# Kernel optimization log

Measured on AMD Instinct MI355X. Metric: run time of the kernel, lower is better.

The kernel has to match this reference:

```python
import jax, jax.numpy as jnp
import numpy as np

D = 1024
H = 16
HS = D // H
DFF = 4 * D
EPS = 1e-5


def setup_inputs() -> dict:
    key = jax.random.key(0)
    ks = jax.random.split(key, 16)
    s_attn = 1.0 / np.sqrt(D)
    x = jax.random.normal(ks[0], (4, 2048, D), dtype=jnp.float32)
    wq = jax.random.normal(ks[1], (H, D, HS), dtype=jnp.float32) * s_attn
    wk = jax.random.normal(ks[2], (H, D, HS), dtype=jnp.float32) * s_attn
    wv = jax.random.normal(ks[3], (H, D, HS), dtype=jnp.float32) * s_attn
    wo = jax.random.normal(ks[4], (D, D), dtype=jnp.float32) * s_attn
    bo = jnp.zeros((D,), dtype=jnp.float32)
    w1 = jax.random.normal(ks[5], (D, DFF), dtype=jnp.float32) * s_attn
    b1 = jnp.zeros((DFF,), dtype=jnp.float32)
    w2 = jax.random.normal(ks[6], (DFF, D), dtype=jnp.float32) * (1.0 / np.sqrt(DFF))
    b2 = jnp.zeros((D,), dtype=jnp.float32)
    g1 = jnp.ones((D,), dtype=jnp.float32)
    be1 = jnp.zeros((D,), dtype=jnp.float32)
    g2 = jnp.ones((D,), dtype=jnp.float32)
    be2 = jnp.zeros((D,), dtype=jnp.float32)
    return {"x": x, "wq": wq, "wk": wk, "wv": wv, "wo": wo, "bo": bo,
            "w1": w1, "b1": b1, "w2": w2, "b2": b2,
            "g1": g1, "be1": be1, "g2": g2, "be2": be2}


def _layernorm(x, g, b):
    mu = jnp.mean(x, axis=-1, keepdims=True)
    var = jnp.mean(jnp.square(x - mu), axis=-1, keepdims=True)
    return (x - mu) * jax.lax.rsqrt(var + EPS) * g + b


def _block(x, wq, wk, wv, wo, bo, w1, b1, w2, b2, g1, be1, g2, be2):
    B, T, C = x.shape
    h = _layernorm(x, g1, be1)
    q = jnp.einsum('btd,hdk->bhtk', h, wq)
    k = jnp.einsum('btd,hdk->bhtk', h, wk)
    v = jnp.einsum('btd,hdk->bhtk', h, wv)
    wei = jnp.einsum('bhtk,bhsk->bhts', q, k) * (HS ** -0.5)
    causal = jnp.tril(jnp.ones((T, T), dtype=bool))
    wei = jnp.where(causal, wei, -jnp.inf)
    wei = jax.nn.softmax(wei, axis=-1)
    attn = jnp.einsum('bhts,bhsk->bhtk', wei, v)  # (B,H,T,HS)
    attn = attn.transpose(0, 2, 1, 3).reshape(B, T, C)  # concat heads
    x = x + attn @ wo + bo
    h2 = _layernorm(x, g2, be2)
    ff = jax.nn.relu(h2 @ w1 + b1) @ w2 + b2
    return x + ff


def reference(x, wq, wk, wv, wo, bo, w1, b1, w2, b2, g1, be1, g2, be2):
    return _block(x, wq, wk, wv, wo, bo, w1, b1, w2, b2, g1, be1, g2, be2)
```

## Files before the change

kernel.cpp:

```cpp
#include <hip/hip_runtime.h>
#include <hip/hip_bf16.h>

#define D_ 1024
#define T_ 2048
#define B_ 4
#define H_ 16
#define HS_ 64
#define DFF_ 4096
#define M_TOT 8192

typedef short s8v __attribute__((ext_vector_type(8)));
typedef float f4v __attribute__((ext_vector_type(4)));

__device__ __forceinline__ void gll16(const void* g, void* l) {
  __builtin_amdgcn_global_load_lds(
      (__attribute__((address_space(1))) void*)(g),
      (__attribute__((address_space(3))) void*)(l), 16, 0, 0);
}

__device__ __forceinline__ short f2b(float f) {
  __hip_bfloat16 h = __float2bfloat16(f);
  short s; __builtin_memcpy(&s, &h, 2); return s;
}

#define VMCNT(N) asm volatile("s_waitcnt vmcnt(" #N ")" ::: "memory")
#define SBAR()  do { __builtin_amdgcn_s_barrier(); __builtin_amdgcn_sched_barrier(0); } while (0)

__global__ __launch_bounds__(256) void transpose_all_kernel(
    const float* __restrict__ wq, const float* __restrict__ wk,
    const float* __restrict__ wv, const float* __restrict__ wo,
    const float* __restrict__ w1, const float* __restrict__ w2,
    __hip_bfloat16* __restrict__ qkvT, __hip_bfloat16* __restrict__ woT,
    __hip_bfloat16* __restrict__ w1T, __hip_bfloat16* __restrict__ w2T) {
  const int bid = blockIdx.x;
  const float* src; __hip_bfloat16* dst;
  int R, C, rb, bx, by;
  if (bid < 3072) {
    int j = bid >> 10, w = bid & 1023;
    src = (j == 0) ? wq : (j == 1) ? wk : wv;
    dst = qkvT; R = 1024; C = 64;
    int z = w >> 6, xy = w & 63;
    bx = xy & 1; by = xy >> 1;
    src += (size_t)z * R * C;
    rb = j * 1024 + z * C;
  } else if (bid < 4096) {
    int w = bid - 3072;
    src = wo; dst = woT; R = 1024; C = 1024; rb = 0;
    bx = w & 31; by = w >> 5;
  } else if (bid < 8192) {
    int w = bid - 4096;
    src = w1; dst = w1T; R = 1024; C = 4096; rb = 0;
    bx = w & 127; by = w >> 7;
  } else {
    int w = bid - 8192;
    src = w2; dst = w2T; R = 4096; C = 1024; rb = 0;
    bx = w & 31; by = w >> 5;
  }
  __shared__ float tile[32][33];
  int c0 = bx * 32, r0 = by * 32;
  int tx = threadIdx.x, ty = threadIdx.y;
#pragma unroll
  for (int i = 0; i < 4; ++i)
    tile[ty + i * 8][tx] = src[(size_t)(r0 + ty + i * 8) * C + c0 + tx];
  __syncthreads();
#pragma unroll
  for (int i = 0; i < 4; ++i)
    dst[(size_t)(rb + c0 + ty + i * 8) * R + r0 + tx] =
        __float2bfloat16(tile[tx][ty + i * 8]);
}

__global__ __launch_bounds__(256) void transpose_v_kernel(
    const __hip_bfloat16* __restrict__ Vb, __hip_bfloat16* __restrict__ Vt) {
  const int bh = blockIdx.y;
  const int t0 = blockIdx.x * 64;
  __shared__ short tile[64][72];
  const int tid = threadIdx.x;
  const int r = tid >> 2, cg = tid & 3;
  const __hip_bfloat16* src = Vb + ((size_t)bh * T_ + t0 + r) * HS_ + cg * 16;
  s8v v0 = *(const s8v*)(src);
  s8v v1 = *(const s8v*)(src + 8);
  *(s8v*)&tile[r][cg * 16] = v0;
  *(s8v*)&tile[r][cg * 16 + 8] = v1;
  __syncthreads();
  const int hs = r;
  short o0[8], o1[8];
#pragma unroll
  for (int k2 = 0; k2 < 8; ++k2) o0[k2] = tile[cg * 16 + k2][hs];
#pragma unroll
  for (int k2 = 0; k2 < 8; ++k2) o1[k2] = tile[cg * 16 + 8 + k2][hs];
  __hip_bfloat16* dst = Vt + ((size_t)bh * HS_ + hs) * T_ + t0 + cg * 16;
  *(s8v*)dst = *(s8v*)o0;
  *(s8v*)(dst + 8) = *(s8v*)o1;
}

__global__ __launch_bounds__(256) void ln_kernel(
    const float* __restrict__ x, const float* __restrict__ g,
    const float* __restrict__ be, __hip_bfloat16* __restrict__ out) {
  int row = blockIdx.x;
  int t = threadIdx.x;
  float4 v = ((const float4*)(x + (size_t)row * D_))[t];
  float s = v.x + v.y + v.z + v.w;
  float ss = v.x * v.x + v.y * v.y + v.z * v.z + v.w * v.w;
#pragma unroll
  for (int o = 1; o < 64; o <<= 1) { s += __shfl_xor(s, o); ss += __shfl_xor(ss, o); }
  __shared__ float rs[4], rss[4];
  int w = t >> 6, l = t & 63;
  if (l == 0) { rs[w] = s; rss[w] = ss; }
  __syncthreads();
  s = rs[0] + rs[1] + rs[2] + rs[3];
  ss = rss[0] + rss[1] + rss[2] + rss[3];
  float mu = s * (1.f / D_);
  float var = ss * (1.f / D_) - mu * mu;
  float r = rsqrtf(var + 1e-5f);
  float4 gv = ((const float4*)g)[t];
  float4 bv = ((const float4*)be)[t];
  union { ushort4 u; __hip_bfloat16 h[4]; } pk;
  pk.h[0] = __float2bfloat16((v.x - mu) * r * gv.x + bv.x);
  pk.h[1] = __float2bfloat16((v.y - mu) * r * gv.y + bv.y);
  pk.h[2] = __float2bfloat16((v.z - mu) * r * gv.z + bv.z);
  pk.h[3] = __float2bfloat16((v.w - mu) * r * gv.w + bv.w);
  ((ushort4*)(out + (size_t)row * D_))[t] = pk.u;
}

__global__ __launch_bounds__(256) void gemm_bt_kernel(
    const __hip_bfloat16* __restrict__ A, const __hip_bfloat16* __restrict__ Bt,
    int M, int N, int K,
    float* __restrict__ p0, const float* __restrict__ bias,
    const float* __restrict__ res) {
  __shared__ short sA[2][128 * 32], sB[2][128 * 32];
  const int gdx = gridDim.x;
  const int nwg = gdx * gridDim.y;
  const int orig = blockIdx.y * gdx + blockIdx.x;
  const int xcd = orig & 7;
  const int c = orig >> 3;
  const int rows = (nwg >> 3) / gdx;
  const int i2 = c & 1;
  const int nn = (c >> 1) % gdx;
  const int gg = (c >> 1) / gdx;
  const int m0 = (xcd * rows + gg * 2 + i2) * 128, n0 = nn * 128;
  const int t = threadIdx.x, l = t & 63, w = t >> 6;
  const int wr = w >> 1, wc = w & 1, lg = l >> 4, lo = l & 15;
  f4v acc[4][4];
#pragma unroll
  for (int m = 0; m < 4; ++m)
#pragma unroll
    for (int n = 0; n < 4; ++n) acc[m][n] = (f4v){0.f, 0.f, 0.f, 0.f};
  const int NT = K >> 5;
  auto stage = [&](int kt, int bi) {
#pragma unroll
    for (int j = 0; j < 2; ++j) {
      int i = j * 256 + t;
      int row = i >> 2, sl = i & 3;
      int ss = sl ^ ((row >> 1) & 3);
      gll16(A + (size_t)(m0 + row) * K + kt * 32 + ss * 8, (char*)sA[bi] + i * 16);
      gll16(Bt + (size_t)(n0 + row) * K + kt * 32 + ss * 8, (char*)sB[bi] + i * 16);
    }
  };
  stage(0, 0);
  stage(1, 1);
  VMCNT(4);
  SBAR();
  for (int kt = 0; kt < NT; ++kt) {
    const int bi = kt & 1;
    s8v af[4], bf[4];
#pragma unroll
    for (int m = 0; m < 4; ++m) {
      int row = wr * 64 + m * 16 + lo;
      int ss = lg ^ ((row >> 1) & 3);
      af[m] = *(const s8v*)((const char*)sA[bi] + row * 64 + ss * 16);
    }
#pragma unroll
    for (int n = 0; n < 4; ++n) {
      int row = wc * 64 + n * 16 + lo;
      int ss = lg ^ ((row >> 1) & 3);
      bf[n] = *(const s8v*)((const char*)sB[bi] + row * 64 + ss * 16);
    }
    __builtin_amdgcn_s_setprio(1);
#pragma unroll
    for (int m = 0; m < 4; ++m)
#pragma unroll
      for (int n = 0; n < 4; ++n)
        acc[m][n] = __builtin_amdgcn_mfma_f32_16x16x32_bf16(af[m], bf[n], acc[m][n], 0, 0, 0);
    __builtin_amdgcn_s_setprio(0);
    if (kt == NT - 1) break;
    SBAR();
    if (kt + 2 < NT) { stage(kt + 2, bi); VMCNT(4); }
    else             { VMCNT(0); }
    SBAR();
  }
#pragma unroll
  for (int mi = 0; mi < 4; ++mi)
#pragma unroll
    for (int j = 0; j < 4; ++j) {
      int mg = m0 + wr * 64 + mi * 16 + lg * 4 + j;
#pragma unroll
      for (int ni = 0; ni < 4; ++ni) {
        int ng = n0 + wc * 64 + ni * 16 + lo;
        p0[(size_t)mg * N + ng] = res[(size_t)mg * N + ng] + acc[mi][ni][j] + bias[ng];
      }
    }
}

template <int EPI>
__global__ __launch_bounds__(512, 2) void gemm_bt_256(
    const __hip_bfloat16* __restrict__ A, const __hip_bfloat16* __restrict__ Bt,
    int M, int N, int K,
    void* __restrict__ p0, void* __restrict__ p1, void* __restrict__ p2,
    const float* __restrict__ bias) {
  __shared__ short sA[2][256 * 32], sB[2][256 * 32];
  const int gdx = gridDim.x;
  const int gdy = gridDim.y;
  const int orig = blockIdx.y * gdx + blockIdx.x;
  const int xcd = orig & 7;
  const int c = orig >> 3;
  const int rowsPerXcd = gdy >> 3;
  const int g = c / (2 * gdx);
  const int r = c % (2 * gdx);
  const int i2 = r & 1, nn = r >> 1;
  const int m0 = (xcd * rowsPerXcd + g * 2 + i2) * 256;
  const int n0 = nn * 256;
  const int t = threadIdx.x, l = t & 63, wid = t >> 6;
  const int wm = wid >> 2, wn = wid & 3, lg = l >> 4, lo = l & 15;
  f4v acc[8][4];
#pragma unroll
  for (int m = 0; m < 8; ++m)
#pragma unroll
    for (int n = 0; n < 4; ++n) acc[m][n] = (f4v){0.f, 0.f, 0.f, 0.f};
  const int NT = K >> 5;
  auto stage = [&](int kt, int bi) {
#pragma unroll
    for (int j = 0; j < 2; ++j) {
      int i = j * 512 + t;
      int row = i >> 2, sl = i & 3;
      int ss = sl ^ ((row >> 1) & 3);
      gll16(A + (size_t)(m0 + row) * K + kt * 32 + ss * 8, (char*)sA[bi] + i * 16);
      gll16(Bt + (size_t)(n0 + row) * K + kt * 32 + ss * 8, (char*)sB[bi] + i * 16);
    }
  };
  stage(0, 0);
  stage(1, 1);
  VMCNT(4);
  SBAR();
  for (int kt = 0; kt < NT; ++kt) {
    const int bi = kt & 1;
    const char* cA = (const char*)sA[bi];
    const char* cB = (const char*)sB[bi];
    s8v bf[4];
#pragma unroll
    for (int nr = 0; nr < 4; ++nr) {
      int row = wn * 64 + nr * 16 + lo;
      int ss = lg ^ ((row >> 1) & 3);
      bf[nr] = *(const s8v*)(cB + row * 64 + ss * 16);
    }
    {
      s8v af[4];
#pragma unroll
      for (int mr = 0; mr < 4; ++mr) {
        int row = wm * 128 + mr * 16 + lo;
        int ss = lg ^ ((row >> 1) & 3);
        af[mr] = *(const s8v*)(cA + row * 64 + ss * 16);
      }
      __builtin_amdgcn_s_setprio(1);
#pragma unroll
      for (int mr = 0; mr < 4; ++mr)
#pragma unroll
        for (int nr = 0; nr < 4; ++nr)
          acc[mr][nr] = __builtin_amdgcn_mfma_f32_16x16x32_bf16(af[mr], bf[nr], acc[mr][nr], 0, 0, 0);
      __builtin_amdgcn_s_setprio(0);
    }
    {
      s8v af[4];
#pragma unroll
      for (int mr = 0; mr < 4; ++mr) {
        int row = wm * 128 + (mr + 4) * 16 + lo;
        int ss = lg ^ ((row >> 1) & 3);
        af[mr] = *(const s8v*)(cA + row * 64 + ss * 16);
      }
      __builtin_amdgcn_s_setprio(1);
#pragma unroll
      for (int mr = 0; mr < 4; ++mr)
#pragma unroll
        for (int nr = 0; nr < 4; ++nr)
          acc[mr + 4][nr] = __builtin_amdgcn_mfma_f32_16x16x32_bf16(af[mr], bf[nr], acc[mr + 4][nr], 0, 0, 0);
      __builtin_amdgcn_s_setprio(0);
    }
    if (kt == NT - 1) break;
    SBAR();
    if (kt + 2 < NT) { stage(kt + 2, bi); VMCNT(4); }
    else             { VMCNT(0); }
    SBAR();
  }
#pragma unroll
  for (int mi = 0; mi < 8; ++mi)
#pragma unroll
    for (int j = 0; j < 4; ++j) {
      int mg = m0 + wm * 128 + mi * 16 + lg * 4 + j;
#pragma unroll
      for (int ni = 0; ni < 4; ++ni) {
        int ng = n0 + wn * 64 + ni * 16 + lo;
        float v = acc[mi][ni][j];
        if constexpr (EPI == 0) {
          int wi = ng >> 10, within = ng & 1023, hh = within >> 6, hs = within & 63;
          __hip_bfloat16* dst = (wi == 0) ? (__hip_bfloat16*)p0
                               : (wi == 1) ? (__hip_bfloat16*)p1
                                           : (__hip_bfloat16*)p2;
          int b = mg >> 11, tt = mg & 2047;
          dst[(((size_t)(b * H_ + hh)) * T_ + tt) * HS_ + hs] = __float2bfloat16(v);
        } else {
          float y = v + bias[ng];
          y = y > 0.f ? y : 0.f;
          ((__hip_bfloat16*)p0)[(size_t)mg * N + ng] = __float2bfloat16(y);
        }
      }
    }
}

template <bool MASK>
__device__ __forceinline__ void attn_step(
    int s0, int qrow, int lg, int lo,
    const short* __restrict__ sKb, const short* __restrict__ sVb,
    short* __restrict__ sPw,
    const s8v (&qf)[2][2], f4v (&acc)[2][4], float (&rsum)[2][4]) {
  s8v kf[4][2];
#pragma unroll
  for (int si = 0; si < 4; ++si) {
    int row = si * 16 + lo;
#pragma unroll
    for (int kc = 0; kc < 2; ++kc) {
      int slot = (kc * 4 + lg) ^ (row & 7);
      kf[si][kc] = *(const s8v*)((const char*)sKb + row * 128 + slot * 16);
    }
  }
  f4v sfr[2][4];
#pragma unroll
  for (int mi = 0; mi < 2; ++mi)
#pragma unroll
    for (int si = 0; si < 4; ++si) {
      sfr[mi][si] = (f4v){0.f, 0.f, 0.f, 0.f};
#pragma unroll
      for (int kc = 0; kc < 2; ++kc)
        sfr[mi][si] = __builtin_amdgcn_mfma_f32_16x16x32_bf16(
            qf[mi][kc], kf[si][kc], sfr[mi][si], 0, 0, 0);
    }
  const float c = 0.18033688f;
  float p[2][4][4];
#pragma unroll
  for (int mi = 0; mi < 2; ++mi)
#pragma unroll
    for (int si = 0; si < 4; ++si)
#pragma unroll
      for (int j = 0; j < 4; ++j) {
        float vv = sfr[mi][si][j] * c;
        if (MASK) {
          int r = qrow + mi * 16 + lg * 4 + j;
          int s = s0 + si * 16 + lo;
          vv = (s <= r) ? vv : -3e38f;
        }
        float e = exp2f(vv);
        p[mi][si][j] = e;
        rsum[mi][j] += e;
      }
#pragma unroll
  for (int mi = 0; mi < 2; ++mi)
#pragma unroll
    for (int si = 0; si < 4; ++si)
#pragma unroll
      for (int j = 0; j < 4; ++j) {
        int row = mi * 16 + lg * 4 + j;
        int s = si * 16 + lo;
        int slot = (s >> 3) ^ (row & 7);
        *(short*)((char*)sPw + row * 128 + slot * 16 + (s & 7) * 2) =
            f2b(p[mi][si][j]);
      }
  s8v pa[2][2], vf[4][2];
#pragma unroll
  for (int mi = 0; mi < 2; ++mi) {
    int row = mi * 16 + lo;
#pragma unroll
    for (int sb = 0; sb < 2; ++sb) {
      int slot = (sb * 4 + lg) ^ (row & 7);
      pa[mi][sb] = *(const s8v*)((const char*)sPw + row * 128 + slot * 16);
    }
  }
#pragma unroll
  for (int ni = 0; ni < 4; ++ni) {
    int row = ni * 16 + lo;
#pragma unroll
    for (int sb = 0; sb < 2; ++sb) {
      int slot = (sb * 4 + lg) ^ (row & 7);
      vf[ni][sb] = *(const s8v*)((const char*)sVb + row * 128 + slot * 16);
    }
  }
#pragma unroll
  for (int mi = 0; mi < 2; ++mi)
#pragma unroll
    for (int ni = 0; ni < 4; ++ni)
#pragma unroll
      for (int sb = 0; sb < 2; ++sb)
        acc[mi][ni] = __builtin_amdgcn_mfma_f32_16x16x32_bf16(
            pa[mi][sb], vf[ni][sb], acc[mi][ni], 0, 0, 0);
}

__global__ __launch_bounds__(256) void attn_kernel(
    const __hip_bfloat16* __restrict__ Q, const __hip_bfloat16* __restrict__ K,
    const __hip_bfloat16* __restrict__ Vt, __hip_bfloat16* __restrict__ O) {
  const int bh = blockIdx.y;
  const int t = threadIdx.x, w = t >> 6, l = t & 63, lg = l >> 4, lo = l & 15;
  const size_t kbase = (size_t)bh * T_ * HS_;
  const size_t vbase = (size_t)bh * HS_ * T_;
  __shared__ short sK[2][64 * 64];
  __shared__ short sV[2][64 * 64];
  __shared__ short sP[4][32 * 64];
  const int b = bh >> 4, hh = bh & 15;
  for (int pass = 0; pass < 2; ++pass) {
    const int tile = pass ? (15 - (int)blockIdx.x) : (int)blockIdx.x;
    const int q0 = tile * 128;
    const int qrow = q0 + w * 32;
    s8v qf[2][2];
#pragma unroll
    for (int mi = 0; mi < 2; ++mi)
#pragma unroll
      for (int kc = 0; kc < 2; ++kc)
        qf[mi][kc] = *(const s8v*)(Q + kbase +
                                   (size_t)(qrow + mi * 16 + lo) * HS_ +
                                   kc * 32 + lg * 8);
    f4v acc[2][4];
    float rsum[2][4];
#pragma unroll
    for (int mi = 0; mi < 2; ++mi) {
#pragma unroll
      for (int ni = 0; ni < 4; ++ni) acc[mi][ni] = (f4v){0.f, 0.f, 0.f, 0.f};
#pragma unroll
      for (int j = 0; j < 4; ++j) rsum[mi][j] = 0.f;
    }
    const int nst = q0 / 64 + 2;
    auto stg = [&](int st) {
      int bi = st & 1;
      int s0 = st * 64;
#pragma unroll
      for (int r = 0; r < 2; ++r) {
        int i = r * 256 + t;
        int row = i >> 3, sl = i & 7;
        int sls = sl ^ (row & 7);
        gll16(K + kbase + (size_t)(s0 + row) * HS_ + sls * 8,
              (char*)sK[bi] + i * 16);
        gll16(Vt + vbase + (size_t)row * T_ + s0 + sls * 8,
              (char*)sV[bi] + i * 16);
      }
    };
    stg(0);
    __syncthreads();
    for (int st = 0; st < nst; ++st) {
      if (st + 1 < nst) stg(st + 1);
      const int s0 = st * 64;
      if (s0 <= qrow + 31) {
        if (st < nst - 2)
          attn_step<false>(s0, qrow, lg, lo, sK[st & 1], sV[st & 1], sP[w],
                           qf, acc, rsum);
        else
          attn_step<true>(s0, qrow, lg, lo, sK[st & 1], sV[st & 1], sP[w],
                          qf, acc, rsum);
      }
      __syncthreads();
    }
#pragma unroll
    for (int mi = 0; mi < 2; ++mi)
#pragma unroll
      for (int j = 0; j < 4; ++j) {
        float rs = rsum[mi][j];
#pragma unroll
        for (int o = 1; o < 16; o <<= 1) rs += __shfl_xor(rs, o);
        int r = qrow + mi * 16 + lg * 4 + j;
        float inv = 1.f / rs;
#pragma unroll
        for (int ni = 0; ni < 4; ++ni) {
          int cc = ni * 16 + lo;
          O[((size_t)b * T_ + r) * D_ + hh * HS_ + cc] =
              __float2bfloat16(acc[mi][ni][j] * inv);
        }
      }
  }
}

extern "C" void kernel_launch(void* const* d_in, const int* in_sizes, int n_in,
                              void* d_out, int out_size, void* d_ws, size_t ws_size,
                              hipStream_t stream) {
  const float* x   = (const float*)d_in[0];
  const float* wq  = (const float*)d_in[1];
  const float* wk  = (const float*)d_in[2];
  const float* wv  = (const float*)d_in[3];
  const float* wo  = (const float*)d_in[4];
  const float* bo  = (const float*)d_in[5];
  const float* w1  = (const float*)d_in[6];
  const float* b1  = (const float*)d_in[7];
  const float* w2  = (const float*)d_in[8];
  const float* b2  = (const float*)d_in[9];
  const float* g1  = (const float*)d_in[10];
  const float* be1 = (const float*)d_in[11];
  const float* g2  = (const float*)d_in[12];
  const float* be2 = (const float*)d_in[13];
  float* out = (float*)d_out;

  char* ws = (char*)d_ws;
  auto alloc = [&](size_t bytes) {
    char* p = ws;
    ws += (bytes + 255) & ~(size_t)255;
    return p;
  };
  __hip_bfloat16* qkvT  = (__hip_bfloat16*)alloc((size_t)3 * D_ * D_ * 2);
  __hip_bfloat16* woT   = (__hip_bfloat16*)alloc((size_t)D_ * D_ * 2);
  __hip_bfloat16* w1T   = (__hip_bfloat16*)alloc((size_t)DFF_ * D_ * 2);
  __hip_bfloat16* w2T   = (__hip_bfloat16*)alloc((size_t)D_ * DFF_ * 2);
  __hip_bfloat16* hbuf  = (__hip_bfloat16*)alloc((size_t)M_TOT * D_ * 2);
  float*          x1    = (float*)alloc((size_t)M_TOT * D_ * 4);
  __hip_bfloat16* Vtb   = (__hip_bfloat16*)x1;
  char* aliased = alloc((size_t)M_TOT * DFF_ * 2);
  __hip_bfloat16* Qb    = (__hip_bfloat16*)(aliased);
  __hip_bfloat16* Kb    = (__hip_bfloat16*)(aliased + (size_t)M_TOT * D_ * 2);
  __hip_bfloat16* Vb    = (__hip_bfloat16*)(aliased + (size_t)M_TOT * D_ * 4);
  __hip_bfloat16* attnb = (__hip_bfloat16*)(aliased + (size_t)M_TOT * D_ * 6);
  __hip_bfloat16* ffb   = (__hip_bfloat16*)(aliased);

  transpose_all_kernel<<<dim3(12288), dim3(32, 8), 0, stream>>>(
      wq, wk, wv, wo, w1, w2, qkvT, woT, w1T, w2T);
  ln_kernel<<<M_TOT, 256, 0, stream>>>(x, g1, be1, hbuf);
  gemm_bt_256<0><<<dim3(12, 32), 512, 0, stream>>>(hbuf, qkvT, M_TOT, 3 * D_, D_,
                                                   Qb, Kb, Vb, nullptr);
  transpose_v_kernel<<<dim3(32, 64), 256, 0, stream>>>(Vb, Vtb);
  attn_kernel<<<dim3(8, 64), 256, 0, stream>>>(Qb, Kb, Vtb, attnb);
  gemm_bt_kernel<<<dim3(8, 64), 256, 0, stream>>>(attnb, woT, M_TOT, D_, D_,
                                                  x1, bo, x);
  ln_kernel<<<M_TOT, 256, 0, stream>>>(x1, g2, be2, hbuf);
  gemm_bt_256<2><<<dim3(16, 32), 512, 0, stream>>>(hbuf, w1T, M_TOT, DFF_, D_,
                                                   ffb, nullptr, nullptr, b1);
  gemm_bt_kernel<<<dim3(8, 64), 256, 0, stream>>>(ffb, w2T, M_TOT, D_, DFF_,
                                                  out, b2, x1);
}
```

Baseline: 544.3 us.

## Triple-buffer GEMM LDS pipeline with one barrier and 128-tile QKV GEMM

Both GEMM kernels move from double to triple LDS buffering. Each k-step now has a single barrier placed before the fragment reads, and the prefetch for step kt+2 is issued right after the MFMAs into the third buffer, replacing the two barriers per iteration. The QKV projection also switches from the 256x256 tile kernel to the 128x128 tile kernel, giving more workgroups (24x64). The cost is extra LDS per block, 48KB for the 256 kernel, which may limit occupancy, and the smaller QKV tile reuses less data.

```diff
diff --git a/kernel.cpp b/kernel.cpp
--- a/kernel.cpp
+++ b/kernel.cpp
@@ -24,7 +24,7 @@
 }
 
 #define VMCNT(N) asm volatile("s_waitcnt vmcnt(" #N ")" ::: "memory")
-#define SBAR()  do { __builtin_amdgcn_s_barrier(); __builtin_amdgcn_sched_barrier(0); } while (0)
+#define BAR() do { __builtin_amdgcn_s_barrier(); asm volatile("" ::: "memory"); } while (0)
 
 __global__ __launch_bounds__(256) void transpose_all_kernel(
     const float* __restrict__ wq, const float* __restrict__ wk,
@@ -122,12 +122,13 @@
   ((ushort4*)(out + (size_t)row * D_))[t] = pk.u;
 }
 
-__global__ __launch_bounds__(256) void gemm_bt_kernel(
+template <int EPI>
+__global__ __launch_bounds__(256) void gemm_bt_128(
     const __hip_bfloat16* __restrict__ A, const __hip_bfloat16* __restrict__ Bt,
     int M, int N, int K,
-    float* __restrict__ p0, const float* __restrict__ bias,
-    const float* __restrict__ res) {
-  __shared__ short sA[2][128 * 32], sB[2][128 * 32];
+    void* __restrict__ p0, void* __restrict__ p1, void* __restrict__ p2,
+    const float* __restrict__ bias, const float* __restrict__ res) {
+  __shared__ short sA[3][128 * 32], sB[3][128 * 32];
   const int gdx = gridDim.x;
   const int nwg = gdx * gridDim.y;
   const int orig = blockIdx.y * gdx + blockIdx.x;
@@ -158,10 +159,10 @@
   };
   stage(0, 0);
   stage(1, 1);
-  VMCNT(4);
-  SBAR();
+  int bi = 0, bs = 2;
   for (int kt = 0; kt < NT; ++kt) {
-    const int bi = kt & 1;
+    if (kt + 1 < NT) { VMCNT(4); } else { VMCNT(0); }
+    BAR();
     s8v af[4], bf[4];
 #pragma unroll
     for (int m = 0; m < 4; ++m) {
@@ -182,11 +183,9 @@
       for (int n = 0; n < 4; ++n)
         acc[m][n] = __builtin_amdgcn_mfma_f32_16x16x32_bf16(af[m], bf[n], acc[m][n], 0, 0, 0);
     __builtin_amdgcn_s_setprio(0);
-    if (kt == NT - 1) break;
-    SBAR();
-    if (kt + 2 < NT) { stage(kt + 2, bi); VMCNT(4); }
-    else             { VMCNT(0); }
-    SBAR();
+    if (kt + 2 < NT) stage(kt + 2, bs);
+    bi = (bi == 2) ? 0 : bi + 1;
+    bs = (bs == 2) ? 0 : bs + 1;
   }
 #pragma unroll
   for (int mi = 0; mi < 4; ++mi)
@@ -196,18 +195,27 @@
 #pragma unroll
       for (int ni = 0; ni < 4; ++ni) {
         int ng = n0 + wc * 64 + ni * 16 + lo;
-        p0[(size_t)mg * N + ng] = res[(size_t)mg * N + ng] + acc[mi][ni][j] + bias[ng];
-      }
-    }
-}
-
-template <int EPI>
+        float v = acc[mi][ni][j];
+        if constexpr (EPI == 0) {
+          int wi = ng >> 10, within = ng & 1023, hh = within >> 6, hs = within & 63;
+          __hip_bfloat16* dst = (wi == 0) ? (__hip_bfloat16*)p0
+                               : (wi == 1) ? (__hip_bfloat16*)p1
+                                           : (__hip_bfloat16*)p2;
+          int b = mg >> 11, tt = mg & 2047;
+          dst[(((size_t)(b * H_ + hh)) * T_ + tt) * HS_ + hs] = __float2bfloat16(v);
+        } else {
+          ((float*)p0)[(size_t)mg * N + ng] =
+              res[(size_t)mg * N + ng] + v + bias[ng];
+        }
+      }
+    }
+}
+
 __global__ __launch_bounds__(512, 2) void gemm_bt_256(
     const __hip_bfloat16* __restrict__ A, const __hip_bfloat16* __restrict__ Bt,
     int M, int N, int K,
-    void* __restrict__ p0, void* __restrict__ p1, void* __restrict__ p2,
-    const float* __restrict__ bias) {
-  __shared__ short sA[2][256 * 32], sB[2][256 * 32];
+    __hip_bfloat16* __restrict__ p0, const float* __restrict__ bias) {
+  __shared__ short sA[3][256 * 32], sB[3][256 * 32];
   const int gdx = gridDim.x;
   const int gdy = gridDim.y;
   const int orig = blockIdx.y * gdx + blockIdx.x;
@@ -239,10 +247,10 @@
   };
   stage(0, 0);
   stage(1, 1);
-  VMCNT(4);
-  SBAR();
+  int bi = 0, bs = 2;
   for (int kt = 0; kt < NT; ++kt) {
-    const int bi = kt & 1;
+    if (kt + 1 < NT) { VMCNT(4); } else { VMCNT(0); }
+    BAR();
     const char* cA = (const char*)sA[bi];
     const char* cB = (const char*)sB[bi];
     s8v bf[4];
@@ -284,11 +292,9 @@
           acc[mr + 4][nr] = __builtin_amdgcn_mfma_f32_16x16x32_bf16(af[mr], bf[nr], acc[mr + 4][nr], 0, 0, 0);
       __builtin_amdgcn_s_setprio(0);
     }
-    if (kt == NT - 1) break;
-    SBAR();
-    if (kt + 2 < NT) { stage(kt + 2, bi); VMCNT(4); }
-    else             { VMCNT(0); }
-    SBAR();
+    if (kt + 2 < NT) stage(kt + 2, bs);
+    bi = (bi == 2) ? 0 : bi + 1;
+    bs = (bs == 2) ? 0 : bs + 1;
   }
 #pragma unroll
   for (int mi = 0; mi < 8; ++mi)
@@ -298,19 +304,9 @@
 #pragma unroll
       for (int ni = 0; ni < 4; ++ni) {
         int ng = n0 + wn * 64 + ni * 16 + lo;
-        float v = acc[mi][ni][j];
-        if constexpr (EPI == 0) {
-          int wi = ng >> 10, within = ng & 1023, hh = within >> 6, hs = within & 63;
-          __hip_bfloat16* dst = (wi == 0) ? (__hip_bfloat16*)p0
-                               : (wi == 1) ? (__hip_bfloat16*)p1
-                                           : (__hip_bfloat16*)p2;
-          int b = mg >> 11, tt = mg & 2047;
-          dst[(((size_t)(b * H_ + hh)) * T_ + tt) * HS_ + hs] = __float2bfloat16(v);
-        } else {
-          float y = v + bias[ng];
-          y = y > 0.f ? y : 0.f;
-          ((__hip_bfloat16*)p0)[(size_t)mg * N + ng] = __float2bfloat16(y);
-        }
+        float y = acc[mi][ni][j] + bias[ng];
+        y = y > 0.f ? y : 0.f;
+        p0[(size_t)mg * N + ng] = __float2bfloat16(y);
       }
     }
 }
@@ -524,15 +520,15 @@
   transpose_all_kernel<<<dim3(12288), dim3(32, 8), 0, stream>>>(
       wq, wk, wv, wo, w1, w2, qkvT, woT, w1T, w2T);
   ln_kernel<<<M_TOT, 256, 0, stream>>>(x, g1, be1, hbuf);
-  gemm_bt_256<0><<<dim3(12, 32), 512, 0, stream>>>(hbuf, qkvT, M_TOT, 3 * D_, D_,
-                                                   Qb, Kb, Vb, nullptr);
+  gemm_bt_128<0><<<dim3(24, 64), 256, 0, stream>>>(hbuf, qkvT, M_TOT, 3 * D_, D_,
+                                                   Qb, Kb, Vb, nullptr, nullptr);
   transpose_v_kernel<<<dim3(32, 64), 256, 0, stream>>>(Vb, Vtb);
   attn_kernel<<<dim3(8, 64), 256, 0, stream>>>(Qb, Kb, Vtb, attnb);
-  gemm_bt_kernel<<<dim3(8, 64), 256, 0, stream>>>(attnb, woT, M_TOT, D_, D_,
-                                                  x1, bo, x);
+  gemm_bt_128<1><<<dim3(8, 64), 256, 0, stream>>>(attnb, woT, M_TOT, D_, D_,
+                                                  x1, nullptr, nullptr, bo, x);
   ln_kernel<<<M_TOT, 256, 0, stream>>>(x1, g2, be2, hbuf);
-  gemm_bt_256<2><<<dim3(16, 32), 512, 0, stream>>>(hbuf, w1T, M_TOT, DFF_, D_,
-                                                   ffb, nullptr, nullptr, b1);
-  gemm_bt_kernel<<<dim3(8, 64), 256, 0, stream>>>(ffb, w2T, M_TOT, D_, DFF_,
-                                                  out, b2, x1);
-}
+  gemm_bt_256<<<dim3(16, 32), 512, 0, stream>>>(hbuf, w1T, M_TOT, DFF_, D_,
+                                                ffb, b1);
+  gemm_bt_128<1><<<dim3(8, 64), 256, 0, stream>>>(ffb, w2T, M_TOT, D_, DFF_,
+                                                  out, nullptr, nullptr, b2, x1);
+}
```

Result: faster. 498.2 us (-8.5%).
